# Kernel tuning notes

Measured on AMD Instinct MI355X. Metric: run time of the kernel, lower is better.

The kernel has to match this reference:

```python
import jax, jax.numpy as jnp
import numpy as np

SHAPE = (128, 128, 128)  # (D, H, W), batch_size = 1
N = 100000               # number of active voxels
CONV_CH = [(3, 64), (64, 64), (64, 96), (96, 96), (96, 128), (128, 128),
           (128, 160), (160, 160), (160, 192), (192, 192), (192, 224),
           (224, 224), (224, 256), (256, 256)]


def _lin(c, shape):
    Sz, Sy, Sx = shape
    return ((c[:, 0] * Sz + c[:, 1]) * Sy + c[:, 2]) * Sx + c[:, 3]


def _subm_pairs(coords, shape):
    # Submanifold conv indice pairs: for each active voxel and each of the
    # 27 kernel offsets, the row index of the active neighbor, or -1.
    Sz, Sy, Sx = shape
    n = coords.shape[0]
    grid = np.full(Sz * Sy * Sx, -1, np.int64)  # batch size 1 dense lookup (like self.grid)
    grid[_lin(coords, shape)] = np.arange(n)
    pairs = []
    for dz in (-1, 0, 1):
        for dy in (-1, 0, 1):
            for dx in (-1, 0, 1):
                z = coords[:, 1] + dz
                y = coords[:, 2] + dy
                x = coords[:, 3] + dx
                ok = (z >= 0) & (z < Sz) & (y >= 0) & (y < Sy) & (x >= 0) & (x < Sx)
                nl = ((coords[:, 0] * Sz + z) * Sy + y) * Sx + x
                pairs.append(np.where(ok, grid[np.clip(nl, 0, grid.size - 1)], -1))
    return np.stack(pairs)  # [27, n]


def _pool_structure(coords, shape):
    # SparseMaxPool3d(2,2): output sites = unique coords//2; inv maps each
    # input voxel to its output window.
    ns = tuple(s // 2 for s in shape)
    c2 = coords.copy()
    c2[:, 1:] = c2[:, 1:] // 2
    key = _lin(c2, ns)
    uniq, inv = np.unique(key, return_inverse=True)
    Sz, Sy, Sx = ns
    b = uniq // (Sz * Sy * Sx)
    r = uniq % (Sz * Sy * Sx)
    z = r // (Sy * Sx)
    r = r % (Sy * Sx)
    nc = np.stack([b, z, r // Sx, r % Sx], 1).astype(np.int64)
    return nc, inv, uniq.shape[0], ns


def _build_plan(coors_np):
    # Paired SubMConv3d layers share an indice_key -> same pairs per level.
    coords = coors_np.astype(np.int64)
    shape = SHAPE
    plan = []
    for lvl in range(7):
        p = jnp.asarray(_subm_pairs(coords, shape))
        plan.append(('conv', p))
        plan.append(('conv', p))
        if lvl < 6:
            coords, inv, m, shape = _pool_structure(coords, shape)
            plan.append(('pool', jnp.asarray(inv), m))
    return plan


def _subm_conv(feats, pairs, W):
    # gather -> GEMM -> accumulate, per kernel offset (W: [27, Cin, Cout])
    out = jnp.zeros((feats.shape[0], W.shape[2]), feats.dtype)
    for k in range(27):
        idx = pairs[k]
        g = jnp.where((idx >= 0)[:, None], feats[jnp.clip(idx, 0)], 0.0)
        out = out + g @ W[k]
    return out


def _forward(feats, weights, plan):
    wi = 0
    for step in plan:
        if step[0] == 'conv':
            feats = _subm_conv(feats, step[1], weights[wi])
            wi += 1
        else:
            feats = jax.ops.segment_max(feats, step[1], num_segments=step[2])
    return feats


def setup_inputs() -> dict:
    rng = np.random.default_rng(0)
    lin = rng.choice(SHAPE[0] * SHAPE[1] * SHAPE[2], size=N, replace=False)
    z = lin // (SHAPE[1] * SHAPE[2])
    r = lin % (SHAPE[1] * SHAPE[2])
    coors = np.stack([np.zeros(N, np.int32), z.astype(np.int32),
                      (r // SHAPE[2]).astype(np.int32), (r % SHAPE[2]).astype(np.int32)], 1)
    key = jax.random.key(0)
    keys = jax.random.split(key, len(CONV_CH) + 1)
    inp = {
        'features': jax.random.normal(keys[0], (N, 3), jnp.float32),
        'coors': jnp.asarray(coors),
        'batch_size': 1,
    }
    for i, (ci, co) in enumerate(CONV_CH):
        inp[f'w{i}'] = jax.random.normal(keys[i + 1], (27, ci, co), jnp.float32) * (1.0 / np.sqrt(27.0 * ci))
    return inp


def reference(features, coors, batch_size, w0, w1, w2, w3, w4, w5, w6, w7, w8, w9, w10, w11, w12, w13):
    plan = _build_plan(np.asarray(coors))
    ws = [w0, w1, w2, w3, w4, w5, w6, w7, w8, w9, w10, w11, w12, w13]
    return _forward(features, ws, plan)
```

## Files before the change

### kernel.cpp

```cpp
#include <hip/hip_runtime.h>
#include <cstdint>
#include <cstddef>


typedef __attribute__((ext_vector_type(8))) short short8v;
typedef __attribute__((ext_vector_type(4))) float f32x4;

static inline int cdiv_h(int a, int b) { return (a + b - 1) / b; }

__device__ inline unsigned short f2bf(float f) {
    unsigned int u = __builtin_bit_cast(unsigned int, f);
    u += 0x7FFFu + ((u >> 16) & 1u);
    return (unsigned short)(u >> 16);
}
__device__ inline float bf2f(unsigned short h) {
    unsigned int u = ((unsigned int)h) << 16;
    return __builtin_bit_cast(float, u);
}

__global__ void set_count_k(int* counts, int n) { counts[0] = n; }

__global__ void scatter_grid_k(const int* __restrict__ coords, const int* __restrict__ cnt,
                               int* __restrict__ grid, int S)
{
    int i = blockIdx.x * blockDim.x + threadIdx.x;
    if (i >= cnt[0]) return;
    int z = coords[i * 4 + 1], y = coords[i * 4 + 2], x = coords[i * 4 + 3];
    grid[(z * S + y) * S + x] = i;
}

__global__ void build_pairs_k(const int* __restrict__ coords, const int* __restrict__ cnt,
                              const int* __restrict__ grid, int* __restrict__ pairs_t, int S)
{
    int i = blockIdx.x * blockDim.x + threadIdx.x;
    if (i >= cnt[0]) return;
    int z = coords[i * 4 + 1], y = coords[i * 4 + 2], x = coords[i * 4 + 3];
    int4* dst = reinterpret_cast<int4*>(pairs_t + (size_t)i * 32);
#pragma unroll
    for (int g = 0; g < 7; ++g) {
        int4 q;
#pragma unroll
        for (int j = 0; j < 4; ++j) {
            int k = g * 4 + j;
            int v = -1;
            if (k < 27) {
                int nz = z + k / 9 - 1;
                int ny = y + (k / 3) % 3 - 1;
                int nx = x + k % 3 - 1;
                if (nz >= 0 && nz < S && ny >= 0 && ny < S && nx >= 0 && nx < S)
                    v = grid[(nz * S + ny) * S + nx];
            }
            ((int*)&q)[j] = v;
        }
        dst[g] = q;
    }
}

struct PackArgs {
    const float* src[13];
    unsigned short* dst[13];
    int cin[13];
    int cout[13];
    int tileStart[14];
};

__global__ __launch_bounds__(256) void pack_all_k(PackArgs pa)
{
    int g = blockIdx.x * 4 + ((int)threadIdx.x >> 6);
    int lane = (int)threadIdx.x & 63;
    if (g >= pa.tileStart[13]) return;
    int li = 0;
    while (li < 12 && g >= pa.tileStart[li + 1]) ++li;
    int tile = g - pa.tileStart[li];
    int CIN = pa.cin[li], COUT = pa.cout[li];
    int NS = CIN >> 5, NT = COUT >> 4;
    int t = tile % NT;
    int s = (tile / NT) % NS;
    int k = tile / (NT * NS);
    int kabs = s * 32 + (lane >> 4) * 8;
    int c = t * 16 + (lane & 15);
    const float* src = pa.src[li] + ((size_t)(k * CIN + kabs)) * COUT + c;
    unsigned short* dst = pa.dst[li] + (size_t)tile * 512 + lane * 8;
#pragma unroll
    for (int j = 0; j < 8; ++j) dst[j] = f2bf(src[(size_t)j * COUT]);
}

__global__ __launch_bounds__(256) void conv0_k(
    const float* __restrict__ fin, const float* __restrict__ W,
    const int* __restrict__ pairs_t, const int* __restrict__ cnt,
    unsigned short* __restrict__ fout)
{
    const int row = blockIdx.x * 16 + ((int)threadIdx.x >> 4);
    const int cg = ((int)threadIdx.x & 15) * 4;
    if (row >= cnt[0]) return;
    float a0 = 0, a1 = 0, a2 = 0, a3 = 0;
    for (int k = 0; k < 27; ++k) {
        int nb = pairs_t[(size_t)row * 32 + k];
        if (nb < 0) continue;
        const float* fr = fin + (size_t)nb * 3;
        const float* wk = W + (size_t)k * 3 * 64 + cg;
#pragma unroll
        for (int ci = 0; ci < 3; ++ci) {
            float f = fr[ci];
            float4 w = *reinterpret_cast<const float4*>(wk + ci * 64);
            a0 += f * w.x; a1 += f * w.y; a2 += f * w.z; a3 += f * w.w;
        }
    }
    size_t o = (size_t)row * 64 + cg;
    fout[o] = f2bf(a0); fout[o + 1] = f2bf(a1);
    fout[o + 2] = f2bf(a2); fout[o + 3] = f2bf(a3);
}

template <int CIN, int COUT, int RT, int CT, bool OUTF32>
__global__ __launch_bounds__(256) void conv_mfma_k(
    const unsigned short* __restrict__ fin, const unsigned short* __restrict__ Wp,
    const int* __restrict__ pairs_t, const int* __restrict__ cnt,
    void* __restrict__ fout)
{
    constexpr int NS = CIN / 32, NT = COUT / 16;
    const int lane = (int)threadIdx.x & 63;
    const int wave = (int)threadIdx.x >> 6;
    const int l15 = lane & 15, lhi = lane >> 4;
    const int M = cnt[0];
    const int rowBase = (blockIdx.x * 4 + wave) * (RT * 16);
    if (rowBase >= M) return;
    const int ct0 = blockIdx.y * CT;

    const unsigned short* __restrict__ finL = fin + (size_t)lhi * 8;
    const unsigned short* __restrict__ WpL  = Wp + (size_t)lane * 8 + (size_t)ct0 * 512;

    f32x4 acc[RT][CT];
#pragma unroll
    for (int a = 0; a < RT; ++a)
#pragma unroll
        for (int b = 0; b < CT; ++b) acc[a][b] = (f32x4){0.f, 0.f, 0.f, 0.f};

    int  rowC[RT];
    bool rOK[RT];
#pragma unroll
    for (int rt = 0; rt < RT; ++rt) {
        int r = rowBase + rt * 16 + l15;
        rOK[rt]  = r < M;
        rowC[rt] = rOK[rt] ? r : (M - 1);
    }

#pragma unroll
    for (int kg = 0; kg < 7; ++kg) {
        int4 nb4[RT];
#pragma unroll
        for (int rt = 0; rt < RT; ++rt) {
            nb4[rt] = *reinterpret_cast<const int4*>(pairs_t + (size_t)rowC[rt] * 32 + kg * 4);
            if (!rOK[rt]) nb4[rt] = make_int4(-1, -1, -1, -1);
        }
#pragma unroll
        for (int j = 0; j < 4; ++j) {
            const int k = kg * 4 + j;
            if (k >= 27) continue;
            int nb[RT];
#pragma unroll
            for (int rt = 0; rt < RT; ++rt)
                nb[rt] = (j == 0) ? nb4[rt].x : (j == 1) ? nb4[rt].y
                       : (j == 2) ? nb4[rt].z : nb4[rt].w;

            int act[RT];
            bool anyAct = false;
#pragma unroll
            for (int rt = 0; rt < RT; ++rt) {
                act[rt] = __any(nb[rt] >= 0);
                anyAct = anyAct || (act[rt] != 0);
            }
            if (!anyAct) continue;

            const unsigned short* wk = WpL + (size_t)k * (NS * NT * 512);
            short8v bfr[NS][CT];
#pragma unroll
            for (int s = 0; s < NS; ++s)
#pragma unroll
                for (int t = 0; t < CT; ++t)
                    bfr[s][t] = *reinterpret_cast<const short8v*>(
                        wk + ((size_t)s * NT + t) * 512);

            short8v afr[NS][RT];
#pragma unroll
            for (int s = 0; s < NS; ++s)
#pragma unroll
                for (int rt = 0; rt < RT; ++rt) {
                    afr[s][rt] = (short8v){};
                    if (nb[rt] >= 0)
                        afr[s][rt] = *reinterpret_cast<const short8v*>(
                            finL + (size_t)nb[rt] * CIN + s * 32);
                }

#pragma unroll
            for (int s = 0; s < NS; ++s)
#pragma unroll
                for (int rt = 0; rt < RT; ++rt) {
                    if (!act[rt]) continue;
#pragma unroll
                    for (int t = 0; t < CT; ++t)
                        acc[rt][t] = __builtin_amdgcn_mfma_f32_16x16x32_bf16(
                            afr[s][rt], bfr[s][t], acc[rt][t], 0, 0, 0);
                }
        }
    }

#pragma unroll
    for (int rt = 0; rt < RT; ++rt) {
#pragma unroll
        for (int j = 0; j < 4; ++j) {
            int r = rowBase + rt * 16 + lhi * 4 + j;
            if (r >= M) continue;
#pragma unroll
            for (int t = 0; t < CT; ++t) {
                int c = (ct0 + t) * 16 + l15;
                if constexpr (OUTF32)
                    ((float*)fout)[(size_t)r * COUT + c] = acc[rt][t][j];
                else
                    ((unsigned short*)fout)[(size_t)r * COUT + c] = f2bf(acc[rt][t][j]);
            }
        }
    }
}

template <int CIN, int COUT, int CTD, int TG>
__global__ __launch_bounds__(64) void conv_deep_k(
    const unsigned short* __restrict__ fin, const unsigned short* __restrict__ Wp,
    const int* __restrict__ pairs_t, const int* __restrict__ cnt,
    float* __restrict__ fout)
{
    constexpr int NS = CIN / 32, NT = COUT / 16;
    const int lane = (int)threadIdx.x;
    const int l15 = lane & 15, lhi = lane >> 4;
    const int M = cnt[0];
    if ((int)blockIdx.x * 16 >= M) return;
    const int row = blockIdx.x * 16 + l15;
    const int ct0 = blockIdx.y * CTD;
    const int k0 = blockIdx.z * TG;

    f32x4 acc[CTD];
#pragma unroll
    for (int t = 0; t < CTD; ++t) acc[t] = (f32x4){0.f, 0.f, 0.f, 0.f};

    bool anyTap = false;
#pragma unroll
    for (int kk = 0; kk < TG; ++kk) {
        const int k = k0 + kk;
        int nb = (row < M) ? pairs_t[(size_t)row * 32 + k] : -1;
        if (!__any(nb >= 0)) continue;
        anyTap = true;
        const unsigned short* wk = Wp + (size_t)k * NS * NT * 512 + (size_t)lane * 8;
#pragma unroll
        for (int s = 0; s < NS; ++s) {
            short8v a = (short8v){};
            if (nb >= 0)
                a = *reinterpret_cast<const short8v*>(
                    fin + (size_t)nb * CIN + s * 32 + lhi * 8);
#pragma unroll
            for (int t = 0; t < CTD; ++t) {
                short8v b = *reinterpret_cast<const short8v*>(
                    wk + ((size_t)s * NT + ct0 + t) * 512);
                acc[t] = __builtin_amdgcn_mfma_f32_16x16x32_bf16(a, b, acc[t], 0, 0, 0);
            }
        }
    }
    if (!anyTap) return;

#pragma unroll
    for (int t = 0; t < CTD; ++t)
#pragma unroll
        for (int j = 0; j < 4; ++j) {
            int r = blockIdx.x * 16 + lhi * 4 + j;
            if (r < M)
                atomicAdd(&fout[(size_t)r * COUT + (ct0 + t) * 16 + l15], acc[t][j]);
        }
}

__global__ __launch_bounds__(256) void f32_to_bf16_k(
    const float* __restrict__ src, const int* __restrict__ cnt,
    unsigned short* __restrict__ dst, int C)
{
    int idx = blockIdx.x * 256 + (int)threadIdx.x;
    if (idx / C >= cnt[0]) return;
    dst[idx] = f2bf(src[idx]);
}

__global__ void mark_occ_k(const int* __restrict__ coords, const int* __restrict__ cnt,
                           int* __restrict__ occ, int Sh)
{
    int i = blockIdx.x * blockDim.x + threadIdx.x;
    if (i >= cnt[0]) return;
    int z = coords[i * 4 + 1] >> 1, y = coords[i * 4 + 2] >> 1, x = coords[i * 4 + 3] >> 1;
    occ[(z * Sh + y) * Sh + x] = 1;
}

__global__ __launch_bounds__(256) void scan_sum_k(const int* __restrict__ occ, int P,
                                                  int* __restrict__ bsum)
{
    int base = blockIdx.x * 4096 + (int)threadIdx.x * 16;
    int s = 0;
#pragma unroll
    for (int j = 0; j < 16; ++j) { int i = base + j; s += (i < P) ? occ[i] : 0; }
    for (int off = 1; off < 64; off <<= 1) s += __shfl_xor(s, off);
    __shared__ int ws[4];
    if ((threadIdx.x & 63) == 0) ws[threadIdx.x >> 6] = s;
    __syncthreads();
    if (threadIdx.x == 0) bsum[blockIdx.x] = ws[0] + ws[1] + ws[2] + ws[3];
}

__global__ void scan_offsets_k(const int* __restrict__ bsum, int nb,
                               int* __restrict__ boff, int* __restrict__ cntOut)
{
    int lane = threadIdx.x;
    int v = (lane < nb) ? bsum[lane] : 0;
    int incl = v;
    for (int off = 1; off < 64; off <<= 1) {
        int t = __shfl_up(incl, off);
        if (lane >= off) incl += t;
    }
    if (lane < nb) boff[lane] = incl - v;
    if (lane == 63) cntOut[0] = incl;
}

__global__ __launch_bounds__(256) void scan_emit_k(const int* __restrict__ occ, int P,
                                                   const int* __restrict__ boff,
                                                   int* __restrict__ newcoords, int Sh)
{
    __shared__ int ws[4];
    int tid = threadIdx.x;
    int base = blockIdx.x * 4096 + tid * 16;
    int v[16];
    int s = 0;
#pragma unroll
    for (int j = 0; j < 16; ++j) { int i = base + j; v[j] = (i < P) ? occ[i] : 0; s += v[j]; }
    int mysum = s;
    int incl = s;
    for (int off = 1; off < 64; off <<= 1) {
        int t = __shfl_up(incl, off);
        if ((tid & 63) >= off) incl += t;
    }
    if ((tid & 63) == 63) ws[tid >> 6] = incl;
    __syncthreads();
    int waveOff = 0;
    for (int w = 0; w < (tid >> 6); ++w) waveOff += ws[w];
    int r = boff[blockIdx.x] + waveOff + incl - mysum;
    const int SS = Sh * Sh;
#pragma unroll
    for (int j = 0; j < 16; ++j) {
        if (v[j]) {
            int c = base + j;
            newcoords[r * 4 + 0] = 0;
            newcoords[r * 4 + 1] = c / SS;
            newcoords[r * 4 + 2] = (c % SS) / Sh;
            newcoords[r * 4 + 3] = c % Sh;
            ++r;
        }
    }
}

__global__ void pool_max_k(const unsigned short* __restrict__ fin, const int* __restrict__ gridPrev,
                           const int* __restrict__ newcoords, const int* __restrict__ cnt,
                           unsigned short* __restrict__ fout, int C, int Sprev)
{
    int idx = blockIdx.x * blockDim.x + threadIdx.x;
    int r = idx / C, c = idx % C;
    if (r >= cnt[0]) return;
    int z2 = newcoords[r * 4 + 1] * 2;
    int y2 = newcoords[r * 4 + 2] * 2;
    int x2 = newcoords[r * 4 + 3] * 2;
    float best = -3.4e38f;
    unsigned short bb = 0;
#pragma unroll
    for (int d = 0; d < 8; ++d) {
        int z = z2 + (d >> 2), y = y2 + ((d >> 1) & 1), x = x2 + (d & 1);
        int j = gridPrev[(z * Sprev + y) * Sprev + x];
        if (j >= 0) {
            unsigned short u = fin[(size_t)j * C + c];
            float f = bf2f(u);
            if (f > best) { best = f; bb = u; }
        }
    }
    fout[(size_t)r * C + c] = bb;
}


template <int CIN, int COUT, int RT, int CT, bool OUTF32>
static void launch_cm(const unsigned short* fin, const unsigned short* Wp,
                      const int* pairs_t, const int* cnt, void* fout,
                      int bound, hipStream_t stream)
{
    constexpr int NT = COUT / 16;
    static_assert(CIN % 32 == 0 && COUT % 16 == 0 && NT % CT == 0, "shape");
    dim3 g(cdiv_h(bound, RT * 64), NT / CT);
    conv_mfma_k<CIN, COUT, RT, CT, OUTF32><<<g, 256, 0, stream>>>(
        fin, Wp, pairs_t, cnt, fout);
}

template <int CIN, int COUT, int CTD, int TG>
static void launch_deep(const unsigned short* fin, const unsigned short* Wp,
                        const int* pairs_t, const int* cnt, float* acc,
                        int bound, hipStream_t stream)
{
    constexpr int NT = COUT / 16;
    static_assert(NT % CTD == 0 && 27 % TG == 0, "shape");
    dim3 g(cdiv_h(bound, 16), NT / CTD, 27 / TG);
    conv_deep_k<CIN, COUT, CTD, TG><<<g, 64, 0, stream>>>(fin, Wp, pairs_t, cnt, acc);
}

extern "C" void kernel_launch(void* const* d_in, const int* in_sizes, int n_in,
                              void* d_out, int out_size, void* d_ws, size_t ws_size,
                              hipStream_t stream)
{
    const float* feats0 = (const float*)d_in[0];
    const int*   coors  = (const int*)d_in[1];
    const float* w[14];
    for (int i = 0; i < 14; ++i) w[i] = (const float*)d_in[3 + i];
    float* out = (float*)d_out;
    const int N = in_sizes[0] / 3;

    char* p = (char*)d_ws;
    int* grid   = (int*)p; p += (size_t)128 * 128 * 128 * 4;
    int* occ    = (int*)p; p += (size_t)64 * 64 * 64 * 4;
    int* counts = (int*)p; p += 256;
    int* bsum   = (int*)p; p += 256;
    int* boff   = (int*)p; p += 256;
    int* pairs_t = (int*)p; p += (size_t)N * 32 * 4;
    int* coordsA = (int*)p; p += (size_t)N * 16;
    int* coordsB = (int*)p; p += (size_t)N * 16;
    unsigned short* featA = (unsigned short*)p; p += (size_t)N * 96 * 2;
    unsigned short* featB = (unsigned short*)p; p += (size_t)N * 96 * 2;
    float* scratch = (float*)p; p += (size_t)4096 * 160 * 4 + 1024;
    unsigned short* wpBase = (unsigned short*)p;

    static const int CH[14][2] = {{3,64},{64,64},{64,96},{96,96},{96,128},{128,128},
                                  {128,160},{160,160},{160,192},{192,192},{192,224},
                                  {224,224},{224,256},{256,256}};
    unsigned short* wp[14];
    PackArgs pa;
    {
        size_t off = 0;
        int ts = 0;
        for (int i = 1; i < 14; ++i) {
            wp[i] = wpBase + off;
            off += (size_t)27 * CH[i][0] * CH[i][1];
            pa.src[i - 1] = w[i];
            pa.dst[i - 1] = wp[i];
            pa.cin[i - 1] = CH[i][0];
            pa.cout[i - 1] = CH[i][1];
            pa.tileStart[i - 1] = ts;
            ts += 27 * (CH[i][0] / 32) * (CH[i][1] / 16);
        }
        pa.tileStart[13] = ts;
    }

    int bounds[7];
    for (int l = 0; l < 7; ++l) {
        int S = 128 >> l, c = S * S * S;
        bounds[l] = N < c ? N : c;
    }

    set_count_k<<<1, 1, 0, stream>>>(counts, N);
    hipMemsetAsync(d_out, 0, (size_t)out_size * 4, stream);
    pack_all_k<<<cdiv_h(pa.tileStart[13], 4), 256, 0, stream>>>(pa);

    auto build_level = [&](const int* coordsL, int lvl) {
        int S = 128 >> lvl;
        hipMemsetAsync(grid, 0xFF, (size_t)S * S * S * 4, stream);
        int blocks = cdiv_h(bounds[lvl], 256);
        scatter_grid_k<<<blocks, 256, 0, stream>>>(coordsL, counts + lvl, grid, S);
        build_pairs_k<<<blocks, 256, 0, stream>>>(coordsL, counts + lvl, grid, pairs_t, S);
    };

    auto do_pool = [&](const int* coordsL, int lvl, const unsigned short* fin,
                       unsigned short* fout, int C, int* coordsOut) {
        int S = 128 >> lvl, Sh = S / 2, P = Sh * Sh * Sh;
        hipMemsetAsync(occ, 0, (size_t)P * 4, stream);
        mark_occ_k<<<cdiv_h(bounds[lvl], 256), 256, 0, stream>>>(coordsL, counts + lvl, occ, Sh);
        int nb = cdiv_h(P, 4096);
        scan_sum_k<<<nb, 256, 0, stream>>>(occ, P, bsum);
        scan_offsets_k<<<1, 64, 0, stream>>>(bsum, nb, boff, counts + lvl + 1);
        scan_emit_k<<<nb, 256, 0, stream>>>(occ, P, boff, coordsOut, Sh);
        int total = bounds[lvl + 1] * C;
        pool_max_k<<<cdiv_h(total, 256), 256, 0, stream>>>(fin, grid, coordsOut,
                                                           counts + lvl + 1, fout, C, S);
    };

    auto deep_conv = [&](auto launcher, const unsigned short* fin, int wi, int lvl,
                         unsigned short* dst, int COUT) {
        hipMemsetAsync(scratch, 0, (size_t)bounds[lvl] * COUT * 4, stream);
        launcher(fin, wp[wi], pairs_t, counts + lvl, scratch, bounds[lvl], stream);
        f32_to_bf16_k<<<cdiv_h(bounds[lvl] * COUT, 256), 256, 0, stream>>>(
            scratch, counts + lvl, dst, COUT);
    };

    build_level(coors, 0);
    conv0_k<<<cdiv_h(bounds[0], 16), 256, 0, stream>>>(feats0, w[0], pairs_t, counts + 0, featA);
    launch_cm<64, 64, 4, 4, false>(featA, wp[1], pairs_t, counts + 0, featB, bounds[0], stream);
    do_pool(coors, 0, featB, featA, 64, coordsA);
    build_level(coordsA, 1);
    launch_cm<64, 96, 4, 3, false>(featA, wp[2], pairs_t, counts + 1, featB, bounds[1], stream);
    launch_cm<96, 96, 4, 3, false>(featB, wp[3], pairs_t, counts + 1, featA, bounds[1], stream);
    do_pool(coordsA, 1, featA, featB, 96, coordsB);
    build_level(coordsB, 2);
    launch_cm<96, 128, 4, 4, false>(featB, wp[4], pairs_t, counts + 2, featA, bounds[2], stream);
    launch_cm<128, 128, 4, 4, false>(featA, wp[5], pairs_t, counts + 2, featB, bounds[2], stream);
    do_pool(coordsB, 2, featB, featA, 128, coordsA);
    build_level(coordsA, 3);
    deep_conv(launch_deep<128, 160, 2, 3>, featA, 6, 3, featB, 160);
    deep_conv(launch_deep<160, 160, 2, 3>, featB, 7, 3, featA, 160);
    do_pool(coordsA, 3, featA, featB, 160, coordsB);
    build_level(coordsB, 4);
    deep_conv(launch_deep<160, 192, 2, 3>, featB, 8, 4, featA, 192);
    deep_conv(launch_deep<192, 192, 2, 3>, featA, 9, 4, featB, 192);
    do_pool(coordsB, 4, featB, featA, 192, coordsA);
    build_level(coordsA, 5);
    deep_conv(launch_deep<192, 224, 1, 1>, featA, 10, 5, featB, 224);
    deep_conv(launch_deep<224, 224, 1, 1>, featB, 11, 5, featA, 224);
    do_pool(coordsA, 5, featA, featB, 224, coordsB);
    build_level(coordsB, 6);
    deep_conv(launch_deep<224, 256, 1, 1>, featB, 12, 6, featA, 256);
    launch_deep<256, 256, 1, 1>(featA, wp[13], pairs_t, counts + 6, out, bounds[6], stream);
}
```

Baseline: 892.2 us.

## Stage conv weights in LDS with double-buffered async loads, full output width per block

Replaces the register-fragment MFMA conv kernel for the shallow levels with one that stages each kernel offset's full weight slab into shared memory, using global_load_lds with a double buffer so the next offset's weights load while the current one computes. Each block now computes all output channels instead of splitting channels across grid.y, so gathered input features are read once per row tile rather than once per channel slice. Row tile per wave drops from 4 to 2 to keep the larger accumulator set in registers. It adds a __syncthreads per offset, per-offset scalar neighbor loads, and large LDS use, all of which can limit occupancy.

```diff
diff --git a/kernel.cpp b/kernel.cpp
--- a/kernel.cpp
+++ b/kernel.cpp
@@ -16,6 +16,12 @@
 __device__ inline float bf2f(unsigned short h) {
     unsigned int u = ((unsigned int)h) << 16;
     return __builtin_bit_cast(float, u);
+}
+
+__device__ inline void gload_lds16(const void* g, void* l) {
+    auto gp = (const __attribute__((address_space(1))) unsigned int*)(uintptr_t)g;
+    auto lp = (__attribute__((address_space(3))) unsigned int*)(uintptr_t)l;
+    __builtin_amdgcn_global_load_lds(gp, lp, 16, 0, 0);
 }
 
 __global__ void set_count_k(int* counts, int n) { counts[0] = n; }
@@ -111,29 +117,29 @@
     fout[o + 2] = f2bf(a2); fout[o + 3] = f2bf(a3);
 }
 
-template <int CIN, int COUT, int RT, int CT, bool OUTF32>
-__global__ __launch_bounds__(256) void conv_mfma_k(
+template <int CIN, int COUT, int RT, bool OUTF32>
+__global__ __launch_bounds__(256) void conv_lds_k(
     const unsigned short* __restrict__ fin, const unsigned short* __restrict__ Wp,
     const int* __restrict__ pairs_t, const int* __restrict__ cnt,
     void* __restrict__ fout)
 {
     constexpr int NS = CIN / 32, NT = COUT / 16;
+    constexpr int NCH = NS * NT;
+    __shared__ unsigned short sB[2][NCH * 512];
+
     const int lane = (int)threadIdx.x & 63;
     const int wave = (int)threadIdx.x >> 6;
     const int l15 = lane & 15, lhi = lane >> 4;
     const int M = cnt[0];
     const int rowBase = (blockIdx.x * 4 + wave) * (RT * 16);
-    if (rowBase >= M) return;
-    const int ct0 = blockIdx.y * CT;
 
     const unsigned short* __restrict__ finL = fin + (size_t)lhi * 8;
-    const unsigned short* __restrict__ WpL  = Wp + (size_t)lane * 8 + (size_t)ct0 * 512;
-
-    f32x4 acc[RT][CT];
+
+    f32x4 acc[RT][NT];
 #pragma unroll
     for (int a = 0; a < RT; ++a)
 #pragma unroll
-        for (int b = 0; b < CT; ++b) acc[a][b] = (f32x4){0.f, 0.f, 0.f, 0.f};
+        for (int b = 0; b < NT; ++b) acc[a][b] = (f32x4){0.f, 0.f, 0.f, 0.f};
 
     int  rowC[RT];
     bool rOK[RT];
@@ -141,45 +147,46 @@
     for (int rt = 0; rt < RT; ++rt) {
         int r = rowBase + rt * 16 + l15;
         rOK[rt]  = r < M;
-        rowC[rt] = rOK[rt] ? r : (M - 1);
-    }
-
-#pragma unroll
-    for (int kg = 0; kg < 7; ++kg) {
-        int4 nb4[RT];
+        rowC[rt] = rOK[rt] ? r : 0;
+    }
+
+#define STAGE(K, BUF)                                                            \
+    {                                                                            \
+        const unsigned short* src =                                              \
+            Wp + (size_t)(K) * (NCH * 512) + (size_t)lane * 8;                   \
+        _Pragma("unroll") for (int idx = wave; idx < NCH; idx += 4)              \
+            gload_lds16(src + (size_t)idx * 512, &sB[BUF][idx * 512]);           \
+    }
+
+    int nbCur[RT], nbNxt[RT];
+#pragma unroll
+    for (int rt = 0; rt < RT; ++rt)
+        nbCur[rt] = rOK[rt] ? pairs_t[(size_t)rowC[rt] * 32 + 0] : -1;
+
+    STAGE(0, 0);
+
+    for (int k = 0; k < 27; ++k) {
+        __syncthreads();
+        if (k < 26) {
+            STAGE(k + 1, (k + 1) & 1);
+#pragma unroll
+            for (int rt = 0; rt < RT; ++rt)
+                nbNxt[rt] = rOK[rt] ? pairs_t[(size_t)rowC[rt] * 32 + (k + 1)] : -1;
+        }
+
+        int nb[RT], act[RT];
+        bool anyAct = false;
 #pragma unroll
         for (int rt = 0; rt < RT; ++rt) {
-            nb4[rt] = *reinterpret_cast<const int4*>(pairs_t + (size_t)rowC[rt] * 32 + kg * 4);
-            if (!rOK[rt]) nb4[rt] = make_int4(-1, -1, -1, -1);
-        }
-#pragma unroll
-        for (int j = 0; j < 4; ++j) {
-            const int k = kg * 4 + j;
-            if (k >= 27) continue;
-            int nb[RT];
-#pragma unroll
-            for (int rt = 0; rt < RT; ++rt)
-                nb[rt] = (j == 0) ? nb4[rt].x : (j == 1) ? nb4[rt].y
-                       : (j == 2) ? nb4[rt].z : nb4[rt].w;
-
-            int act[RT];
-            bool anyAct = false;
-#pragma unroll
-            for (int rt = 0; rt < RT; ++rt) {
-                act[rt] = __any(nb[rt] >= 0);
-                anyAct = anyAct || (act[rt] != 0);
-            }
-            if (!anyAct) continue;
-
-            const unsigned short* wk = WpL + (size_t)k * (NS * NT * 512);
-            short8v bfr[NS][CT];
-#pragma unroll
-            for (int s = 0; s < NS; ++s)
-#pragma unroll
-                for (int t = 0; t < CT; ++t)
-                    bfr[s][t] = *reinterpret_cast<const short8v*>(
-                        wk + ((size_t)s * NT + t) * 512);
-
+            nb[rt] = nbCur[rt];
+            act[rt] = __any(nb[rt] >= 0);
+            anyAct = anyAct || (act[rt] != 0);
+        }
+#pragma unroll
+        for (int rt = 0; rt < RT; ++rt) nbCur[rt] = nbNxt[rt];
+
+        if (anyAct) {
+            const unsigned short* __restrict__ buf = sB[k & 1];
             short8v afr[NS][RT];
 #pragma unroll
             for (int s = 0; s < NS; ++s)
@@ -190,19 +197,22 @@
                         afr[s][rt] = *reinterpret_cast<const short8v*>(
                             finL + (size_t)nb[rt] * CIN + s * 32);
                 }
-
 #pragma unroll
             for (int s = 0; s < NS; ++s)
 #pragma unroll
                 for (int rt = 0; rt < RT; ++rt) {
                     if (!act[rt]) continue;
 #pragma unroll
-                    for (int t = 0; t < CT; ++t)
+                    for (int t = 0; t < NT; ++t) {
+                        short8v b = *reinterpret_cast<const short8v*>(
+                            &buf[(s * NT + t) * 512 + lane * 8]);
                         acc[rt][t] = __builtin_amdgcn_mfma_f32_16x16x32_bf16(
-                            afr[s][rt], bfr[s][t], acc[rt][t], 0, 0, 0);
+                            afr[s][rt], b, acc[rt][t], 0, 0, 0);
+                    }
                 }
         }
     }
+#undef STAGE
 
 #pragma unroll
     for (int rt = 0; rt < RT; ++rt) {
@@ -211,8 +221,8 @@
             int r = rowBase + rt * 16 + lhi * 4 + j;
             if (r >= M) continue;
 #pragma unroll
-            for (int t = 0; t < CT; ++t) {
-                int c = (ct0 + t) * 16 + l15;
+            for (int t = 0; t < NT; ++t) {
+                int c = t * 16 + l15;
                 if constexpr (OUTF32)
                     ((float*)fout)[(size_t)r * COUT + c] = acc[rt][t][j];
                 else
@@ -383,16 +393,14 @@
 }
 
 
-template <int CIN, int COUT, int RT, int CT, bool OUTF32>
-static void launch_cm(const unsigned short* fin, const unsigned short* Wp,
+template <int CIN, int COUT, int RT, bool OUTF32>
+static void launch_cl(const unsigned short* fin, const unsigned short* Wp,
                       const int* pairs_t, const int* cnt, void* fout,
                       int bound, hipStream_t stream)
 {
-    constexpr int NT = COUT / 16;
-    static_assert(CIN % 32 == 0 && COUT % 16 == 0 && NT % CT == 0, "shape");
-    dim3 g(cdiv_h(bound, RT * 64), NT / CT);
-    conv_mfma_k<CIN, COUT, RT, CT, OUTF32><<<g, 256, 0, stream>>>(
-        fin, Wp, pairs_t, cnt, fout);
+    static_assert(CIN % 32 == 0 && COUT % 16 == 0, "shape");
+    dim3 g(cdiv_h(bound, RT * 64));
+    conv_lds_k<CIN, COUT, RT, OUTF32><<<g, 256, 0, stream>>>(fin, Wp, pairs_t, cnt, fout);
 }
 
 template <int CIN, int COUT, int CTD, int TG>
@@ -494,15 +502,15 @@
 
     build_level(coors, 0);
     conv0_k<<<cdiv_h(bounds[0], 16), 256, 0, stream>>>(feats0, w[0], pairs_t, counts + 0, featA);
-    launch_cm<64, 64, 4, 4, false>(featA, wp[1], pairs_t, counts + 0, featB, bounds[0], stream);
+    launch_cl<64, 64, 2, false>(featA, wp[1], pairs_t, counts + 0, featB, bounds[0], stream);
     do_pool(coors, 0, featB, featA, 64, coordsA);
     build_level(coordsA, 1);
-    launch_cm<64, 96, 4, 3, false>(featA, wp[2], pairs_t, counts + 1, featB, bounds[1], stream);
-    launch_cm<96, 96, 4, 3, false>(featB, wp[3], pairs_t, counts + 1, featA, bounds[1], stream);
+    launch_cl<64, 96, 2, false>(featA, wp[2], pairs_t, counts + 1, featB, bounds[1], stream);
+    launch_cl<96, 96, 2, false>(featB, wp[3], pairs_t, counts + 1, featA, bounds[1], stream);
     do_pool(coordsA, 1, featA, featB, 96, coordsB);
     build_level(coordsB, 2);
-    launch_cm<96, 128, 4, 4, false>(featB, wp[4], pairs_t, counts + 2, featA, bounds[2], stream);
-    launch_cm<128, 128, 4, 4, false>(featA, wp[5], pairs_t, counts + 2, featB, bounds[2], stream);
+    launch_cl<96, 128, 2, false>(featB, wp[4], pairs_t, counts + 2, featA, bounds[2], stream);
+    launch_cl<128, 128, 2, false>(featA, wp[5], pairs_t, counts + 2, featB, bounds[2], stream);
     do_pool(coordsB, 2, featB, featA, 128, coordsA);
     build_level(coordsA, 3);
     deep_conv(launch_deep<128, 160, 2, 3>, featA, 6, 3, featB, 160);
```

After: 745.0 us. -16.5%, faster.
